# Performance work log

Measured on AMD Instinct MI355X. Metric: run time of the kernel, lower is better.

## Reference

```python
import jax, jax.numpy as jnp
import numpy as np

NB = 56  # numblock
EPS = 1e-5


def layer_norm(x, w, b):
    mu = jnp.mean(x, axis=-1, keepdims=True)
    var = jnp.mean(jnp.square(x - mu), axis=-1, keepdims=True)
    return (x - mu) * jax.lax.rsqrt(var + EPS) * w + b


def min_gru(x, w_hg, w_out):
    # lucidrains minGRU, log-space Heinsen parallel scan (seq_len > 1 branch)
    hg = x @ w_hg                      # [n, L, 2*di]
    hidden, gate = jnp.split(hg, 2, axis=-1)
    log_coeffs = -jax.nn.softplus(gate)        # log(1 - z)
    log_z = -jax.nn.softplus(-gate)            # log z
    # log_g(hidden): where(h>=0, log(relu(h)+0.5), -softplus(-h))
    log_tilde_h = jnp.where(hidden >= 0,
                            jnp.log(jax.nn.relu(hidden) + 0.5),
                            -jax.nn.softplus(-hidden))
    log_values = log_z + log_tilde_h
    a_star = jnp.cumsum(log_coeffs, axis=1)
    log_h = a_star + jax.lax.cumlogsumexp(log_values - a_star, axis=1)
    return jnp.exp(log_h) @ w_out      # [n, L, dim]


def block_fwd(x, norm_w, norm_b, dw_w, dw_b, gru1_whg, gru1_wout,
              gru2_whg, gru2_wout, norm2_w, norm2_b, p1_w, p1_b, p2_w, p2_b):
    n, L, dim = x.shape
    residual = x
    h = layer_norm(x, norm_w, norm_b)
    # depthwise 3x3 conv on [n, dim, NB, NB]
    img = h.reshape(n, NB, NB, dim).transpose(0, 3, 1, 2)
    img = jax.lax.conv_general_dilated(
        img, dw_w, window_strides=(1, 1), padding='SAME',
        feature_group_count=dim,
        dimension_numbers=('NCHW', 'OIHW', 'NCHW')) + dw_b[None, :, None, None]
    h = img.reshape(n, dim, L).transpose(0, 2, 1)
    # bidirectional minGRU: second branch on 2D-flipped sequence
    h2 = jnp.flip(h.reshape(n, NB, NB, dim), axis=(1, 2)).reshape(n, L, dim)
    x1 = min_gru(h, gru1_whg, gru1_wout)
    x2 = jnp.flip(min_gru(h2, gru2_whg, gru2_wout), axis=1)
    h = x1 + x2 + residual
    residual = h
    m = layer_norm(h, norm2_w, norm2_b)
    m = jax.nn.gelu(m @ p1_w + p1_b, approximate=False)
    m = m @ p2_w + p2_b
    return m + residual


def setup_inputs():
    key = jax.random.key(0)
    ks = jax.random.split(key, 9)
    n, dim = 16, 384
    di = 2 * dim          # expansion_factor=2
    mlp = 4 * dim         # mlp_ratio=4
    L = NB * NB

    def w(k, shape, s=0.02):
        return jax.random.normal(k, shape, jnp.float32) * s

    return {
        'x': jax.random.normal(ks[0], (n, L, dim), jnp.float32),
        'norm_w': jnp.ones((dim,), jnp.float32),
        'norm_b': jnp.zeros((dim,), jnp.float32),
        'dw_w': w(ks[1], (dim, 1, 3, 3), 0.1),
        'dw_b': jnp.zeros((dim,), jnp.float32),
        'gru1_whg': w(ks[2], (dim, 2 * di)),
        'gru1_wout': w(ks[3], (di, dim)),
        'gru2_whg': w(ks[4], (dim, 2 * di)),
        'gru2_wout': w(ks[5], (di, dim)),
        'norm2_w': jnp.ones((dim,), jnp.float32),
        'norm2_b': jnp.zeros((dim,), jnp.float32),
        'p1_w': w(ks[6], (dim, mlp)),
        'p1_b': jnp.zeros((mlp,), jnp.float32),
        'p2_w': w(ks[7], (mlp, dim)),
        'p2_b': jnp.zeros((dim,), jnp.float32),
    }


def reference(x, norm_w, norm_b, dw_w, dw_b, gru1_whg, gru1_wout,
              gru2_whg, gru2_wout, norm2_w, norm2_b, p1_w, p1_b, p2_w, p2_b):
    return block_fwd(x, norm_w, norm_b, dw_w, dw_b, gru1_whg, gru1_wout,
                     gru2_whg, gru2_wout, norm2_w, norm2_b, p1_w, p1_b, p2_w, p2_b)
```

## Files before the change

kernel.cpp:

```cpp
#include <hip/hip_runtime.h>
#include <hip/hip_bf16.h>

typedef __hip_bfloat16 bf16;
typedef __attribute__((ext_vector_type(8))) short short8;
typedef __attribute__((ext_vector_type(4))) short short4v;
typedef __attribute__((ext_vector_type(4))) float floatx4;

#define N_BATCH 16
#define NBQ 56
#define SEQ (NBQ*NBQ)
#define DIM 384
#define DI 768
#define MROWS (N_BATCH*SEQ)
#define NSEG 49
#define SEGLEN 64

__device__ __forceinline__ float b2f(bf16 v){ return __bfloat162float(v); }
__device__ __forceinline__ bf16 f2b(float v){ return __float2bfloat16(v); }

__device__ __forceinline__ float ldin(const void* p, size_t i, int f32){
    return f32 ? ((const float*)p)[i] : __bfloat162float(((const bf16*)p)[i]);
}
__device__ __forceinline__ void stout(void* p, size_t i, int f32, float v){
    if (f32) ((float*)p)[i] = v; else ((bf16*)p)[i] = __float2bfloat16(v);
}

__device__ __forceinline__ void gl2lds16(const void* g, void* l) {
    __builtin_amdgcn_global_load_lds((const __attribute__((address_space(1))) void*)g,
                                     (__attribute__((address_space(3))) void*)l, 16, 0, 0);
}

__global__ void detect_kernel(const unsigned short* __restrict__ x, int* __restrict__ flag) {
    __shared__ int cnt;
    if (threadIdx.x == 0) cnt = 0;
    __syncthreads();
    int c = 0;
    for (int i = threadIdx.x; i < 16384; i += 256) {
        unsigned short u = x[i];
        if ((u & 0x7F80) == 0x7F80) ++c;
    }
    if (c) atomicAdd(&cnt, c);
    __syncthreads();
    if (threadIdx.x == 0) *flag = cnt ? 1 : 0;
}

__global__ __launch_bounds__(64) void ln_kernel(const void* __restrict__ x,
        const void* __restrict__ w, const void* __restrict__ b,
        bf16* __restrict__ y, size_t row_off, const int* __restrict__ flag) {
    const int f32 = *flag;
    const size_t row = row_off + blockIdx.x;
    const int lane = threadIdx.x;
    float v[6]; float s = 0.f;
    #pragma unroll
    for (int j = 0; j < 6; ++j) { v[j] = ldin(x, row*DIM + lane + j*64, f32); s += v[j]; }
    #pragma unroll
    for (int o = 32; o; o >>= 1) s += __shfl_xor(s, o);
    const float mu = s * (1.f/DIM);
    float s2 = 0.f;
    #pragma unroll
    for (int j = 0; j < 6; ++j) { float d = v[j]-mu; s2 += d*d; }
    #pragma unroll
    for (int o = 32; o; o >>= 1) s2 += __shfl_xor(s2, o);
    const float inv = rsqrtf(s2*(1.f/DIM) + 1e-5f);
    bf16* yr = y + (size_t)blockIdx.x * DIM;
    #pragma unroll
    for (int j = 0; j < 6; ++j) {
        int c = lane + j*64;
        yr[c] = f2b((v[j]-mu)*inv*ldin(w, c, f32) + ldin(b, c, f32));
    }
}

__device__ __forceinline__ floatx4 ld_tok4(const bf16* p){
    short4v s = *(const short4v*)p;
    floatx4 f;
    #pragma unroll
    for (int k = 0; k < 4; ++k) {
        unsigned int u = ((unsigned int)(unsigned short)s[k]) << 16;
        f[k] = __uint_as_float(u);
    }
    return f;
}

__global__ __launch_bounds__(192) void dwconv_kernel(const bf16* __restrict__ h,
        const void* __restrict__ w, const void* __restrict__ bias,
        bf16* __restrict__ out, const int* __restrict__ flag) {
    const int f32 = *flag;
    const int tid = threadIdx.x;
    const int c4  = tid % 96;
    const int j   = blockIdx.x*2 + tid/96;
    const int i0  = blockIdx.y*8;
    const int n   = blockIdx.z;
    const int c0  = c4*4;
    const bf16* hn = h + (size_t)n*SEQ*DIM + c0;

    floatx4 wgt[9];
    #pragma unroll
    for (int t = 0; t < 9; ++t)
        #pragma unroll
        for (int k = 0; k < 4; ++k)
            wgt[t][k] = ldin(w, (size_t)(c0+k)*9 + t, f32);
    floatx4 bv;
    #pragma unroll
    for (int k = 0; k < 4; ++k) bv[k] = ldin(bias, c0+k, f32);

    const floatx4 zero = (floatx4){0.f,0.f,0.f,0.f};
    floatx4 win[3][3];
    #pragma unroll
    for (int dj = 0; dj < 3; ++dj) {
        const int jj = j + dj - 1;
        const bool jok = (unsigned)jj < NBQ;
        win[0][dj] = (jok && i0 > 0) ? ld_tok4(hn + ((size_t)((i0-1)*NBQ + jj))*DIM) : zero;
        win[1][dj] =  jok            ? ld_tok4(hn + ((size_t)( i0   *NBQ + jj))*DIM) : zero;
    }
    bf16* on = out + (size_t)n*SEQ*DIM + c0;
    #pragma unroll
    for (int r = 0; r < 8; ++r) {
        const int i = i0 + r;
        #pragma unroll
        for (int dj = 0; dj < 3; ++dj) {
            const int jj = j + dj - 1;
            const bool ok = ((unsigned)jj < NBQ) && (i+1 < NBQ);
            win[2][dj] = ok ? ld_tok4(hn + ((size_t)((i+1)*NBQ + jj))*DIM) : zero;
        }
        floatx4 acc = bv;
        #pragma unroll
        for (int di = 0; di < 3; ++di)
            #pragma unroll
            for (int dj = 0; dj < 3; ++dj)
                #pragma unroll
                for (int k = 0; k < 4; ++k)
                    acc[k] += win[di][dj][k] * wgt[di*3+dj][k];
        short4v o;
        #pragma unroll
        for (int k = 0; k < 4; ++k) { bf16 t = f2b(acc[k]); o[k] = *(short*)&t; }
        *(short4v*)(on + ((size_t)(i*NBQ + j))*DIM) = o;
        #pragma unroll
        for (int dj = 0; dj < 3; ++dj) { win[0][dj] = win[1][dj]; win[1][dj] = win[2][dj]; }
    }
}

__global__ __launch_bounds__(64) void scan_p1(const bf16* __restrict__ G,
        float* __restrict__ Aseg, float* __restrict__ Bseg, int dir) {
    const int c = blockIdx.x*64 + threadIdx.x;
    const int s = blockIdx.y;
    const int n = blockIdx.z;
    const bf16* base = G + (size_t)n*SEQ*(2*DI) + c;
    float A = 1.f, B = 0.f;
    #pragma unroll 4
    for (int u = 0; u < SEGLEN; ++u) {
        const int t = dir ? (SEQ-1 - (s*SEGLEN + u)) : (s*SEGLEN + u);
        const bf16* p = base + (size_t)t*(2*DI);
        float hid = b2f(p[0]), gate = b2f(p[DI]);
        float z  = 1.f/(1.f + __expf(-gate));
        float tl = hid >= 0.f ? hid + 0.5f : 1.f/(1.f + __expf(-hid));
        float a = 1.f - z;
        A *= a;
        B = a*B + z*tl;
    }
    const size_t idx = ((size_t)n*NSEG + s)*DI + c;
    Aseg[idx] = A; Bseg[idx] = B;
}

__global__ __launch_bounds__(64) void scan_p2(const float* __restrict__ Aseg,
        const float* __restrict__ Bseg, float* __restrict__ Pseg) {
    const int c = blockIdx.x*64 + threadIdx.x;
    const int n = blockIdx.y;
    float P = 0.f;
    for (int s = 0; s < NSEG; ++s) {
        const size_t idx = ((size_t)n*NSEG + s)*DI + c;
        Pseg[idx] = P;
        P = Aseg[idx]*P + Bseg[idx];
    }
}

__global__ __launch_bounds__(64) void scan_p3(bf16* __restrict__ G,
        const float* __restrict__ Pseg, int dir) {
    const int c = blockIdx.x*64 + threadIdx.x;
    const int s = blockIdx.y;
    const int n = blockIdx.z;
    bf16* base = G + (size_t)n*SEQ*(2*DI) + c;
    float h = Pseg[((size_t)n*NSEG + s)*DI + c];
    #pragma unroll 4
    for (int u = 0; u < SEGLEN; ++u) {
        const int t = dir ? (SEQ-1 - (s*SEGLEN + u)) : (s*SEGLEN + u);
        bf16* p = base + (size_t)t*(2*DI);
        float hid = b2f(p[0]), gate = b2f(p[DI]);
        float z  = 1.f/(1.f + __expf(-gate));
        float tl = hid >= 0.f ? hid + 0.5f : 1.f/(1.f + __expf(-hid));
        h = (1.f - z)*h + z*tl;
        p[0] = f2b(h);
    }
}

__global__ void transpose_kernel(const void* __restrict__ src, bf16* __restrict__ dst,
                                 int R, int C, const int* __restrict__ flag) {
    const int f32 = *flag;
    int idx = blockIdx.x*256 + threadIdx.x;
    if (idx >= R*C) return;
    int r = idx / C, c = idx - r*C;
    dst[(size_t)c*R + r] = f2b(ldin(src, idx, f32));
}

template<int MODE>
__global__ __launch_bounds__(256, 2) void gemm_kernel(
        const bf16* __restrict__ A, int lda,
        const bf16* __restrict__ Bt,
        void* __restrict__ C, int ldc, int K, size_t row_off,
        const void* __restrict__ bias, const void* __restrict__ resid,
        const int* __restrict__ flag) {
    __shared__ __align__(16) short lsA[128*64];
    __shared__ __align__(16) short lsB[128*64];
    const int tid  = threadIdx.x;
    const int tn0  = blockIdx.x * 128;
    const int tm0  = blockIdx.y * 128;
    const int lane = tid & 63;
    const int wave = tid >> 6;
    const int wm = (wave & 1) * 64;
    const int wn = (wave >> 1) * 64;
    const int row16 = lane & 15;
    const int quad  = lane >> 4;
    const int r7    = row16 & 7;

    floatx4 acc[4][4];
    #pragma unroll
    for (int i = 0; i < 4; ++i)
        #pragma unroll
        for (int j = 0; j < 4; ++j)
            acc[i][j] = (floatx4){0.f, 0.f, 0.f, 0.f};

    const int so_row = tid >> 3;
    const int so_pb  = tid & 7;
    const int so_lb  = so_pb ^ (so_row & 7);

    for (int k0 = 0; k0 < K; k0 += 64) {
        const char* Ab = (const char*)(A + (size_t)tm0*lda + k0);
        const char* Bb = (const char*)(Bt + (size_t)tn0*K + k0);
        #pragma unroll
        for (int it = 0; it < 4; ++it) {
            int row = it*32 + so_row;
            gl2lds16(Ab + (size_t)row*((size_t)lda*2) + so_lb*16,
                     (char*)lsA + row*128 + so_pb*16);
        }
        #pragma unroll
        for (int it = 0; it < 4; ++it) {
            int row = it*32 + so_row;
            gl2lds16(Bb + (size_t)row*((size_t)K*2) + so_lb*16,
                     (char*)lsB + row*128 + so_pb*16);
        }
        __syncthreads();
        #pragma unroll
        for (int kk = 0; kk < 64; kk += 32) {
            const int lb = (kk >> 3) + quad;
            const int pb = (lb ^ r7) * 8;
            short8 af[4], bfr[4];
            #pragma unroll
            for (int i = 0; i < 4; ++i)
                af[i] = *(const short8*)(lsA + (wm + i*16 + row16)*64 + pb);
            #pragma unroll
            for (int j = 0; j < 4; ++j)
                bfr[j] = *(const short8*)(lsB + (wn + j*16 + row16)*64 + pb);
            #pragma unroll
            for (int i = 0; i < 4; ++i)
                #pragma unroll
                for (int j = 0; j < 4; ++j)
                    acc[i][j] = __builtin_amdgcn_mfma_f32_16x16x32_bf16(af[i], bfr[j], acc[i][j], 0, 0, 0);
        }
        __syncthreads();
    }

    const int f32 = (MODE == 0) ? 0 : *flag;
    #pragma unroll
    for (int i = 0; i < 4; ++i) {
        #pragma unroll
        for (int j = 0; j < 4; ++j) {
            #pragma unroll
            for (int r = 0; r < 4; ++r) {
                const int gm = tm0 + wm + i*16 + quad*4 + r;
                const int gn = tn0 + wn + j*16 + row16;
                float v = acc[i][j][r];
                if (MODE == 0) {
                    ((bf16*)C)[(size_t)gm*ldc + gn] = f2b(v);
                } else if (MODE == 1) {
                    size_t gi = (row_off + gm)*(size_t)ldc + gn;
                    v += ldin(resid, gi, f32);
                    stout(C, gi, f32, v);
                } else if (MODE == 2) {
                    v += ldin(bias, gn, f32);
                    v = 0.5f*v*(1.f + erff(v*0.70710678118f));
                    ((bf16*)C)[(size_t)gm*ldc + gn] = f2b(v);
                } else {
                    size_t gi = (row_off + gm)*(size_t)ldc + gn;
                    v += ldin(bias, gn, f32) + ldin(resid, gi, f32);
                    stout(C, gi, f32, v);
                }
            }
        }
    }
}

extern "C" void kernel_launch(void* const* d_in, const int* in_sizes, int n_in,
                              void* d_out, int out_size, void* d_ws, size_t ws_size,
                              hipStream_t stream) {
    const void* x       = d_in[0];
    const void* norm_w  = d_in[1];
    const void* norm_b  = d_in[2];
    const void* dw_w    = d_in[3];
    const void* dw_b    = d_in[4];
    const void* whg1    = d_in[5];
    const void* wout1   = d_in[6];
    const void* whg2    = d_in[7];
    const void* wout2   = d_in[8];
    const void* norm2_w = d_in[9];
    const void* norm2_b = d_in[10];
    const void* p1_w    = d_in[11];
    const void* p1_b    = d_in[12];
    const void* p2_w    = d_in[13];
    const void* p2_b    = d_in[14];
    void* out = d_out;
    char* ws = (char*)d_ws;

    const size_t WSZ = 5898240;

    int CH = 16;
    for (;;) {
        size_t need = 256 + WSZ + (size_t)CH * SEQ * 4608;
        if (need <= ws_size || CH == 2) break;
        CH >>= 1;
    }
    const int NC = N_BATCH / CH;
    const int CHROWS = CH * SEQ;

    int* flag = (int*)ws;
    char* wb = ws + 256;
    bf16* WhgT1  = (bf16*)(wb);
    bf16* WhgT2  = (bf16*)(wb + 1179648);
    bf16* WoutT1 = (bf16*)(wb + 2359296);
    bf16* WoutT2 = (bf16*)(wb + 2949120);
    bf16* P1T    = (bf16*)(wb + 3538944);
    bf16* P2T    = (bf16*)(wb + 4718592);
    char* dyn = ws + 256 + WSZ;
    bf16* h_ln_c   = (bf16*)(dyn);
    bf16* h_conv_c = (bf16*)(dyn + (size_t)CHROWS*DIM*2);
    bf16* Gbuf     = (bf16*)(dyn + 2*(size_t)CHROWS*DIM*2);
    bf16* mid_ln_c = h_ln_c;
    float* Aseg = (float*)h_ln_c;
    float* Bseg = Aseg + (size_t)CH*NSEG*DI;
    float* Pseg = Bseg + (size_t)CH*NSEG*DI;

    detect_kernel<<<1, 256, 0, stream>>>((const unsigned short*)x, flag);

    transpose_kernel<<<(384*1536+255)/256, 256, 0, stream>>>(whg1, WhgT1, 384, 1536, flag);
    transpose_kernel<<<(384*1536+255)/256, 256, 0, stream>>>(whg2, WhgT2, 384, 1536, flag);
    transpose_kernel<<<(768*384+255)/256, 256, 0, stream>>>(wout1, WoutT1, 768, 384, flag);
    transpose_kernel<<<(768*384+255)/256, 256, 0, stream>>>(wout2, WoutT2, 768, 384, flag);
    transpose_kernel<<<(384*1536+255)/256, 256, 0, stream>>>(p1_w, P1T, 384, 1536, flag);
    transpose_kernel<<<(1536*384+255)/256, 256, 0, stream>>>(p2_w, P2T, 1536, 384, flag);

    for (int pass = 0; pass < 2; ++pass) {
        const bf16* WhgT  = pass ? WhgT2  : WhgT1;
        const bf16* WoutT = pass ? WoutT2 : WoutT1;
        for (int ck = 0; ck < NC; ++ck) {
            const size_t roff = (size_t)ck * CHROWS;
            if (pass == 0 || NC > 1) {
                ln_kernel<<<CHROWS, 64, 0, stream>>>(x, norm_w, norm_b, h_ln_c, roff, flag);
                dwconv_kernel<<<dim3(28, 7, CH), 192, 0, stream>>>(h_ln_c, dw_w, dw_b, h_conv_c, flag);
            }
            gemm_kernel<0><<<dim3(1536/128, CHROWS/128), 256, 0, stream>>>(
                h_conv_c, DIM, WhgT, Gbuf, 2*DI, DIM, 0, nullptr, nullptr, flag);
            scan_p1<<<dim3(12, NSEG, CH), 64, 0, stream>>>(Gbuf, Aseg, Bseg, pass);
            scan_p2<<<dim3(12, CH), 64, 0, stream>>>(Aseg, Bseg, Pseg);
            scan_p3<<<dim3(12, NSEG, CH), 64, 0, stream>>>(Gbuf, Pseg, pass);
            const void* resid = pass ? (const void*)out : x;
            gemm_kernel<1><<<dim3(DIM/128, CHROWS/128), 256, 0, stream>>>(
                Gbuf, 2*DI, WoutT, out, DIM, DI, roff, nullptr, resid, flag);
        }
    }

    for (int ck = 0; ck < NC; ++ck) {
        const size_t roff = (size_t)ck * CHROWS;
        ln_kernel<<<CHROWS, 64, 0, stream>>>(out, norm2_w, norm2_b, mid_ln_c, roff, flag);
        gemm_kernel<2><<<dim3(1536/128, CHROWS/128), 256, 0, stream>>>(
            mid_ln_c, DIM, P1T, Gbuf, 1536, DIM, 0, p1_b, nullptr, flag);
        gemm_kernel<3><<<dim3(DIM/128, CHROWS/128), 256, 0, stream>>>(
            Gbuf, 1536, P2T, out, DIM, 1536, roff, p2_b, out, flag);
    }
}
```

Measured before the change: 1.153 ms.

## Double-buffer GEMM LDS tiles and remap workgroups across XCDs

The GEMM kernel now uses two LDS buffers per operand, so the global-to-LDS load of the next K tile is issued before the MFMA work on the current tile, and one barrier per iteration is dropped. It also remaps block IDs so that consecutive tiles land on the same XCD, which should improve L2 reuse. LDS use doubles to 64KB per block, which may reduce occupancy below the two blocks per CU asked for in the launch bounds. There is also a possible race if the async LDS loads are not fenced before the barrier.

Result: slower. 1.317 ms (+14.3%).

```diff
diff --git a/kernel.cpp b/kernel.cpp
--- a/kernel.cpp
+++ b/kernel.cpp
@@ -208,11 +208,20 @@
         void* __restrict__ C, int ldc, int K, size_t row_off,
         const void* __restrict__ bias, const void* __restrict__ resid,
         const int* __restrict__ flag) {
-    __shared__ __align__(16) short lsA[128*64];
-    __shared__ __align__(16) short lsB[128*64];
+    __shared__ __align__(16) short lsA[2][128*64];
+    __shared__ __align__(16) short lsB[2][128*64];
     const int tid  = threadIdx.x;
-    const int tn0  = blockIdx.x * 128;
-    const int tm0  = blockIdx.y * 128;
+
+    const int nwg = gridDim.x * gridDim.y;
+    int bid = blockIdx.y * gridDim.x + blockIdx.x;
+    {
+        const int q = nwg >> 3, r = nwg & 7;
+        const int xcd = bid & 7, ix = bid >> 3;
+        bid = (xcd < r ? xcd*(q+1) : r*(q+1) + (xcd-r)*q) + ix;
+    }
+    const int tn0  = (bid % gridDim.x) * 128;
+    const int tm0  = (bid / gridDim.x) * 128;
+
     const int lane = tid & 63;
     const int wave = tid >> 6;
     const int wm = (wave & 1) * 64;
@@ -232,22 +241,34 @@
     const int so_pb  = tid & 7;
     const int so_lb  = so_pb ^ (so_row & 7);
 
-    for (int k0 = 0; k0 < K; k0 += 64) {
-        const char* Ab = (const char*)(A + (size_t)tm0*lda + k0);
-        const char* Bb = (const char*)(Bt + (size_t)tn0*K + k0);
+    const char* Abase = (const char*)A + (size_t)tm0*((size_t)lda*2);
+    const char* Bbase = (const char*)Bt + (size_t)tn0*((size_t)K*2);
+    const int nt = K >> 6;
+
+    auto stage = [&](int buf, int t) {
+        const char* Ab = Abase + (size_t)t*128;
+        const char* Bb = Bbase + (size_t)t*128;
         #pragma unroll
         for (int it = 0; it < 4; ++it) {
             int row = it*32 + so_row;
             gl2lds16(Ab + (size_t)row*((size_t)lda*2) + so_lb*16,
-                     (char*)lsA + row*128 + so_pb*16);
+                     (char*)(lsA[buf]) + row*128 + so_pb*16);
         }
         #pragma unroll
         for (int it = 0; it < 4; ++it) {
             int row = it*32 + so_row;
             gl2lds16(Bb + (size_t)row*((size_t)K*2) + so_lb*16,
-                     (char*)lsB + row*128 + so_pb*16);
-        }
-        __syncthreads();
+                     (char*)(lsB[buf]) + row*128 + so_pb*16);
+        }
+    };
+
+    stage(0, 0);
+    __syncthreads();
+    int cur = 0;
+    for (int t = 0; t < nt; ++t) {
+        if (t + 1 < nt) stage(cur ^ 1, t + 1);
+        const short* la = lsA[cur];
+        const short* lb_ = lsB[cur];
         #pragma unroll
         for (int kk = 0; kk < 64; kk += 32) {
             const int lb = (kk >> 3) + quad;
@@ -255,17 +276,17 @@
             short8 af[4], bfr[4];
             #pragma unroll
             for (int i = 0; i < 4; ++i)
-                af[i] = *(const short8*)(lsA + (wm + i*16 + row16)*64 + pb);
+                af[i] = *(const short8*)(la + (wm + i*16 + row16)*64 + pb);
             #pragma unroll
             for (int j = 0; j < 4; ++j)
-                bfr[j] = *(const short8*)(lsB + (wn + j*16 + row16)*64 + pb);
+                bfr[j] = *(const short8*)(lb_ + (wn + j*16 + row16)*64 + pb);
             #pragma unroll
             for (int i = 0; i < 4; ++i)
                 #pragma unroll
                 for (int j = 0; j < 4; ++j)
                     acc[i][j] = __builtin_amdgcn_mfma_f32_16x16x32_bf16(af[i], bfr[j], acc[i][j], 0, 0, 0);
         }
-        __syncthreads();
+        if (t + 1 < nt) { __syncthreads(); cur ^= 1; }
     }
 
     const int f32 = (MODE == 0) ? 0 : *flag;
```
